# Optimization experiments

Measured on AMD Instinct MI355X. Metric: run time of the kernel, lower is better.

The kernel has to match this reference:

```python
import jax, jax.numpy as jnp
import numpy as np

EPS = 1e-5

def _ln(x, g, b):
    m = jnp.mean(x, -1, keepdims=True)
    v = jnp.mean((x - m) ** 2, -1, keepdims=True)
    return (x - m) * jax.lax.rsqrt(v + EPS) * g + b

def _lstm(x, Wih, Whh, bih, bhh):
    # x: [B, T, D]; torch gate order i, f, g, o; h0 = c0 = 0
    B = x.shape[0]
    H = Whh.shape[1]
    h0 = jnp.zeros((B, H), x.dtype)
    c0 = jnp.zeros((B, H), x.dtype)
    bias = bih + bhh
    def step(carry, xt):
        h, c = carry
        gates = xt @ Wih.T + h @ Whh.T + bias  # [B, 4H]
        i, f, g, o = jnp.split(gates, 4, axis=-1)
        c = jax.nn.sigmoid(f) * c + jax.nn.sigmoid(i) * jnp.tanh(g)
        h = jax.nn.sigmoid(o) * jnp.tanh(c)
        return (h, c), h
    _, hs = jax.lax.scan(step, (h0, c0), jnp.swapaxes(x, 0, 1))
    return jnp.swapaxes(hs, 0, 1)  # [B, T, H]

def setup_inputs() -> dict:
    key = jax.random.key(0)
    ks = jax.random.split(key, 20)
    N, C, F, T = 4, 64, 256, 256
    D, H = 128, 32  # LSTM in/out
    s = 0.05
    inp = {
        "inputs": jax.random.normal(ks[0], (N, C, F, T, 2), jnp.float32),
        "ln1_g": jnp.ones((D,), jnp.float32), "ln1_b": jnp.zeros((D,), jnp.float32),
        "Wih_q": s * jax.random.normal(ks[1], (4 * H, D), jnp.float32),
        "Whh_q": s * jax.random.normal(ks[2], (4 * H, H), jnp.float32),
        "bih_q": s * jax.random.normal(ks[3], (4 * H,), jnp.float32),
        "bhh_q": s * jax.random.normal(ks[4], (4 * H,), jnp.float32),
        "Wih_k": s * jax.random.normal(ks[5], (4 * H, D), jnp.float32),
        "Whh_k": s * jax.random.normal(ks[6], (4 * H, H), jnp.float32),
        "bih_k": s * jax.random.normal(ks[7], (4 * H,), jnp.float32),
        "bhh_k": s * jax.random.normal(ks[8], (4 * H,), jnp.float32),
        "Wih_v": s * jax.random.normal(ks[9], (4 * H, D), jnp.float32),
        "Whh_v": s * jax.random.normal(ks[10], (4 * H, H), jnp.float32),
        "bih_v": s * jax.random.normal(ks[11], (4 * H,), jnp.float32),
        "bhh_v": s * jax.random.normal(ks[12], (4 * H,), jnp.float32),
        "ln2_g": jnp.ones((H,), jnp.float32), "ln2_b": jnp.zeros((H,), jnp.float32),
        "Wr": s * jax.random.normal(ks[13], (C, H // 2), jnp.float32),
        "br": s * jax.random.normal(ks[14], (C,), jnp.float32),
        "Wi": s * jax.random.normal(ks[15], (C, H // 2), jnp.float32),
        "bi": s * jax.random.normal(ks[16], (C,), jnp.float32),
        "ln3_g": jnp.ones((C,), jnp.float32), "ln3_b": jnp.zeros((C,), jnp.float32),
        "prelu_a": jnp.full((1,), 0.25, jnp.float32),
    }
    return inp

def reference(inputs, ln1_g, ln1_b,
              Wih_q, Whh_q, bih_q, bhh_q,
              Wih_k, Whh_k, bih_k, bhh_k,
              Wih_v, Whh_v, bih_v, bhh_v,
              ln2_g, ln2_b, Wr, br, Wi, bi,
              ln3_g, ln3_b, prelu_a):
    N, C, F, T, ri = inputs.shape
    # [N,C,F,T,2] -> [N*F, T, C, 2] -> concat real/imag -> [N*F, T, 2C]
    x4 = jnp.transpose(inputs, (0, 2, 3, 1, 4)).reshape(N * F, T, C, ri)
    x = jnp.concatenate([x4[..., 0], x4[..., 1]], axis=-1)  # [B, T, 128]
    # Self_Attention_T_RICAT (single head)
    xn = _ln(x, ln1_g, ln1_b)
    q = _lstm(xn, Wih_q, Whh_q, bih_q, bhh_q)  # [B, T, 32]
    k = _lstm(xn, Wih_k, Whh_k, bih_k, bhh_k)
    v = _lstm(xn, Wih_v, Whh_v, bih_v, bhh_v)
    energy = jnp.einsum('btf,bsf->bts', q, k) / 4.0  # / 16**0.5
    mask = jnp.tril(jnp.ones((T, T), x.dtype))
    attn = jax.nn.softmax(energy * mask, axis=-1)  # multiplicative mask, as in source
    wv = jnp.einsum('bts,bsf->btf', attn, v)  # [B, T, 32]
    out = _ln(wv, ln2_g, ln2_b)
    # complex-valued linear fusion
    xr, xi = jnp.split(out, 2, axis=-1)  # [B, T, 16] each
    lr_r = xr @ Wr.T + br
    li_i = xi @ Wi.T + bi
    lr_i = xi @ Wr.T + br
    li_r = xr @ Wi.T + bi
    out_real = (lr_r - li_i).reshape(N, F, T, C).transpose(0, 3, 1, 2)  # [N,C,F,T]
    out_imag = (lr_i + li_r).reshape(N, F, T, C).transpose(0, 3, 1, 2)
    outs = jnp.stack([out_real, out_imag], axis=-1)  # [N,C,F,T,2]
    outs_t = jnp.swapaxes(outs, 1, 4)  # [N,2,F,T,C]
    outs = jnp.swapaxes(_ln(outs_t, ln3_g, ln3_b), 1, 4)
    outs = jnp.where(outs >= 0, outs, prelu_a[0] * outs)  # PReLU (eval mode, dropout=identity)
    return outs + inputs
```

## Files before the change

### kernel.cpp

```cpp
#include <hip/hip_runtime.h>
#include <hip/hip_bf16.h>
#include <stddef.h>


typedef __bf16 bf16x8 __attribute__((ext_vector_type(8)));
typedef float f32x4 __attribute__((ext_vector_type(4)));

__device__ __forceinline__ ushort f2bf(float x) {
    uint u = __builtin_bit_cast(uint, x);
    uint r = (u + 0x7fffu + ((u >> 16) & 1u)) >> 16;
    return (ushort)r;
}

__device__ __forceinline__ float fsig(float x) {
    return __builtin_amdgcn_rcpf(1.f + __expf(-x));
}
__device__ __forceinline__ float ftanh(float x) {
    return 1.f - 2.f * __builtin_amdgcn_rcpf(__expf(2.f * x) + 1.f);
}
__device__ __forceinline__ float wredsum(float v) {
#pragma unroll
    for (int off = 32; off; off >>= 1) v += __shfl_xor(v, off);
    return v;
}
__device__ __forceinline__ float hredsum(float v) {
#pragma unroll
    for (int off = 16; off; off >>= 1) v += __shfl_xor(v, off);
    return v;
}

__global__ __launch_bounds__(256) void k_prep(const float* __restrict__ in,
                                              const float* __restrict__ g1,
                                              const float* __restrict__ b1,
                                              ushort* __restrict__ xn) {
    __shared__ float xl[32][129];
    const int n = blockIdx.z, f = blockIdx.y, t0 = blockIdx.x * 32;
    const int tid = threadIdx.x;
    const int c = tid >> 2, q = tid & 3;
    const float* src = in + ((size_t)(n * 64 + c) * 256 + f) * 512 + t0 * 2 + q * 16;
#pragma unroll
    for (int e = 0; e < 4; ++e) {
        float4 v4 = *(const float4*)(src + e * 4);
        int dt = q * 8 + e * 2;
        xl[dt][c]          = v4.x;
        xl[dt][c + 64]     = v4.y;
        xl[dt + 1][c]      = v4.z;
        xl[dt + 1][c + 64] = v4.w;
    }
    __syncthreads();
    const int lane = tid & 63, w = tid >> 6;
    const int b = n * 256 + f;
#pragma unroll 1
    for (int r = 0; r < 8; ++r) {
        int dt = w * 8 + r;
        float a = xl[dt][lane], bb = xl[dt][lane + 64];
        float s = wredsum(a + bb);
        float mean = s * 0.0078125f;
        float da = a - mean, db = bb - mean;
        float var = wredsum(da * da + db * db) * 0.0078125f;
        float inv = __builtin_amdgcn_rsqf(var + 1e-5f);
        size_t base = ((size_t)b * 256 + (t0 + dt)) * 128;
        xn[base + lane]      = f2bf(da * inv * g1[lane] + b1[lane]);
        xn[base + lane + 64] = f2bf(db * inv * g1[lane + 64] + b1[lane + 64]);
    }
}

__global__ __launch_bounds__(256) void k_gemm(const ushort* __restrict__ xn,
                                              const float* __restrict__ Wq,
                                              const float* __restrict__ Wk,
                                              const float* __restrict__ Wv,
                                              const float* __restrict__ bihq, const float* __restrict__ bhhq,
                                              const float* __restrict__ bihk, const float* __restrict__ bhhk,
                                              const float* __restrict__ bihv, const float* __restrict__ bhhv,
                                              ushort* __restrict__ gx) {
    __shared__ ushort a_lds[128 * 136];
    __shared__ ushort w_lds[128 * 136];
    const int tid = threadIdx.x;
    const int m0 = blockIdx.x * 128;

#pragma unroll
    for (int p = 0; p < 8; ++p) {
        int idx = p * 256 + tid;
        int r = idx >> 4, c = idx & 15;
        *(uint4*)&a_lds[r * 136 + c * 8] =
            *(const uint4*)(xn + (size_t)(m0 + r) * 128 + c * 8);
    }

    const int w = tid >> 6, lane = tid & 63;
    const int wr = w >> 1, wc = w & 1;
    const int row16 = lane & 15, koct = lane >> 4;

#pragma unroll 1
    for (int l = 0; l < 3; ++l) {
        const float* W   = (l == 0) ? Wq   : (l == 1) ? Wk   : Wv;
        const float* bih = (l == 0) ? bihq : (l == 1) ? bihk : bihv;
        const float* bhh = (l == 0) ? bhhq : (l == 1) ? bhhk : bhhv;
        __syncthreads();
#pragma unroll
        for (int p = 0; p < 8; ++p) {
            int idx = p * 256 + tid;
            int r = idx >> 4, c = idx & 15;
            const float* wp = W + (size_t)r * 128 + c * 8;
            float4 wa = *(const float4*)wp;
            float4 wb = *(const float4*)(wp + 4);
            union { ushort u[8]; uint4 v; } pk;
            pk.u[0] = f2bf(wa.x); pk.u[1] = f2bf(wa.y); pk.u[2] = f2bf(wa.z); pk.u[3] = f2bf(wa.w);
            pk.u[4] = f2bf(wb.x); pk.u[5] = f2bf(wb.y); pk.u[6] = f2bf(wb.z); pk.u[7] = f2bf(wb.w);
            *(uint4*)&w_lds[r * 136 + c * 8] = pk.v;
        }
        __syncthreads();

        f32x4 acc[4][4];
#pragma unroll
        for (int mi = 0; mi < 4; ++mi)
#pragma unroll
            for (int ni = 0; ni < 4; ++ni) acc[mi][ni] = (f32x4){0.f, 0.f, 0.f, 0.f};

#pragma unroll
        for (int ki = 0; ki < 4; ++ki) {
            bf16x8 af[4], bfr[4];
#pragma unroll
            for (int mi = 0; mi < 4; ++mi)
                af[mi] = *(const bf16x8*)&a_lds[(wr * 64 + mi * 16 + row16) * 136 + ki * 32 + koct * 8];
#pragma unroll
            for (int ni = 0; ni < 4; ++ni)
                bfr[ni] = *(const bf16x8*)&w_lds[(wc * 64 + ni * 16 + row16) * 136 + ki * 32 + koct * 8];
#pragma unroll
            for (int mi = 0; mi < 4; ++mi)
#pragma unroll
                for (int ni = 0; ni < 4; ++ni)
                    acc[mi][ni] = __builtin_amdgcn_mfma_f32_16x16x32_bf16(af[mi], bfr[ni], acc[mi][ni], 0, 0, 0);
        }
        __syncthreads();

#pragma unroll
        for (int ni = 0; ni < 4; ++ni) {
            int g = wc * 64 + ni * 16 + row16;
            float bsv = bih[g] + bhh[g];
            int j = g & 31, gi = g >> 5;
            int s = j * 4 + gi;
#pragma unroll
            for (int mi = 0; mi < 4; ++mi)
#pragma unroll
                for (int q = 0; q < 4; ++q) {
                    int ml = wr * 64 + mi * 16 + koct * 4 + q;
                    w_lds[ml * 136 + s] = f2bf(acc[mi][ni][q] + bsv);
                }
        }
        __syncthreads();
#pragma unroll
        for (int p = 0; p < 8; ++p) {
            int idx = p * 256 + tid;
            int r = idx >> 4, cchunk = idx & 15;
            *(uint4*)&gx[(size_t)(m0 + r) * 384 + l * 128 + cchunk * 8] =
                *(const uint4*)&w_lds[r * 136 + cchunk * 8];
        }
    }
}

__global__ __launch_bounds__(128, 1) void k_lstm(const ushort* __restrict__ gx,
                                                 const float* __restrict__ Whq,
                                                 const float* __restrict__ Whk,
                                                 const float* __restrict__ Whv,
                                                 ushort* __restrict__ qkv) {
    __shared__ ushort H[2][16][40];
    const int tid = threadIdx.x;
    const int w = tid >> 6, lane = tid & 63;
    const int r16 = lane & 15, koct = lane >> 4;
    const int l = blockIdx.x >> 6, bgrp = blockIdx.x & 63;
    const int b = bgrp * 16 + r16;
    const float* Wh = (l == 0) ? Whq : (l == 1) ? Whk : Whv;

    bf16x8 wf[4];
#pragma unroll
    for (int gg = 0; gg < 4; ++gg) {
        int g = 4 * w + gg;
        int jA = 8 * (r16 >> 2) + g;
        int giA = r16 & 3;
        const float* wp = Wh + (size_t)(giA * 32 + jA) * 32 + koct * 8;
        float4 wa = *(const float4*)wp;
        float4 wb = *(const float4*)(wp + 4);
        union { ushort u[8]; bf16x8 v; } pk;
        pk.u[0] = f2bf(wa.x); pk.u[1] = f2bf(wa.y); pk.u[2] = f2bf(wa.z); pk.u[3] = f2bf(wa.w);
        pk.u[4] = f2bf(wb.x); pk.u[5] = f2bf(wb.y); pk.u[6] = f2bf(wb.z); pk.u[7] = f2bf(wb.w);
        wf[gg] = pk.v;
    }

    const ushort* gp = gx + (size_t)b * 98304 + l * 128 + koct * 32 + w * 16;
    uint4 pf[4][2];
#pragma unroll
    for (int tt = 0; tt < 4; ++tt) {
        pf[tt][0] = *(const uint4*)(gp + (size_t)tt * 384);
        pf[tt][1] = *(const uint4*)(gp + (size_t)tt * 384 + 8);
    }

    for (int i = tid; i < 320; i += 128) ((uint*)&H[0][0][0])[i] = 0;
    __syncthreads();

    float cst[4] = {0.f, 0.f, 0.f, 0.f};
    ushort* outp = qkv + ((size_t)(l * 1024 + b)) * 8192 + koct * 8 + w * 4;

#pragma unroll 4
    for (int t = 0; t < 256; ++t) {
        const int sl = t & 3;
        const int p = t & 1;
        bf16x8 hf = *(const bf16x8*)&H[p][r16][koct * 8];

        uint u[8];
        u[0] = pf[sl][0].x; u[1] = pf[sl][0].y; u[2] = pf[sl][0].z; u[3] = pf[sl][0].w;
        u[4] = pf[sl][1].x; u[5] = pf[sl][1].y; u[6] = pf[sl][1].z; u[7] = pf[sl][1].w;
        pf[sl][0] = *(const uint4*)(gp + (size_t)(t + 4) * 384);
        pf[sl][1] = *(const uint4*)(gp + (size_t)(t + 4) * 384 + 8);

        f32x4 acc[4];
#pragma unroll
        for (int gg = 0; gg < 4; ++gg)
#pragma unroll
            for (int q = 0; q < 4; ++q) {
                int v = gg * 4 + q;
                uint w32 = u[v >> 1];
                acc[gg][q] = __builtin_bit_cast(float, (v & 1) ? (w32 & 0xffff0000u) : (w32 << 16));
            }
#pragma unroll
        for (int gg = 0; gg < 4; ++gg)
            acc[gg] = __builtin_amdgcn_mfma_f32_16x16x32_bf16(wf[gg], hf, acc[gg], 0, 0, 0);

        float hv[4];
#pragma unroll
        for (int gg = 0; gg < 4; ++gg) {
            float gi = acc[gg][0], gf = acc[gg][1], gg2 = acc[gg][2], go = acc[gg][3];
            float cN = fsig(gf) * cst[gg] + fsig(gi) * ftanh(gg2);
            cst[gg] = cN;
            hv[gg] = fsig(go) * ftanh(cN);
        }
        uint2 hp;
        __asm__ volatile("v_cvt_pk_bf16_f32 %0, %1, %2" : "=v"(hp.x) : "v"(hv[0]), "v"(hv[1]));
        __asm__ volatile("v_cvt_pk_bf16_f32 %0, %1, %2" : "=v"(hp.y) : "v"(hv[2]), "v"(hv[3]));
        *(uint2*)&H[p ^ 1][r16][koct * 8 + w * 4] = hp;
        *(uint2*)(outp + (size_t)t * 32) = hp;
        __syncthreads();
    }
}

__global__ __launch_bounds__(256) void k_attn(const ushort* __restrict__ qkvb,
                                              float* __restrict__ wvout) {
    __shared__ ushort k_sw[256 * 32];
    __shared__ ushort vt_sw[32 * 256];
    __shared__ ushort p_sw[4][16 * 256];
    const int tid = threadIdx.x, w = tid >> 6, lane = tid & 63;
    const int b = blockIdx.x;
    const ushort* qb = qkvb + (size_t)b * 8192;
    const ushort* kb = qkvb + 8388608 + (size_t)b * 8192;
    const ushort* vb = qkvb + 16777216 + (size_t)b * 8192;
#pragma unroll
    for (int p = 0; p < 4; ++p) {
        int idx = p * 256 + tid;
        int s = idx >> 2, cc = idx & 3;
        uint4 kv = *(const uint4*)(kb + s * 32 + cc * 8);
        int cK = cc ^ ((s >> 1) & 3);
        *(uint4*)&k_sw[s * 32 + cK * 8] = kv;
        uint4 vv = *(const uint4*)(vb + s * 32 + cc * 8);
        union { uint4 v; ushort u[8]; } un; un.v = vv;
#pragma unroll
        for (int e = 0; e < 8; ++e) {
            int row = cc * 8 + e;
            vt_sw[row * 256 + (((s >> 3) ^ (row & 7)) << 3) + (s & 7)] = un.u[e];
        }
    }
    __syncthreads();
    const int r16 = lane & 15, koct = lane >> 4;
    ushort* pw = p_sw[w];
    bf16x8 qf[4];
#pragma unroll
    for (int i = 0; i < 4; ++i) {
        int t = (w * 4 + i) * 16 + r16;
        qf[i] = *(const bf16x8*)(qb + t * 32 + koct * 8);
    }
#pragma unroll 1
    for (int i = 0; i < 4; ++i) {
        const int tb = (w * 4 + i) * 16;
        f32x4 acc[16];
#pragma unroll
        for (int st = 0; st < 16; ++st) acc[st] = (f32x4){0.f, 0.f, 0.f, 0.f};
#pragma unroll
        for (int st = 0; st < 16; ++st) {
            int s = st * 16 + r16;
            int cK = koct ^ ((s >> 1) & 3);
            bf16x8 kf = *(const bf16x8*)&k_sw[s * 32 + cK * 8];
            acc[st] = __builtin_amdgcn_mfma_f32_16x16x32_bf16(qf[i], kf, acc[st], 0, 0, 0);
        }
        float mx[4] = {-1e30f, -1e30f, -1e30f, -1e30f};
#pragma unroll
        for (int st = 0; st < 16; ++st) {
            int s = st * 16 + r16;
#pragma unroll
            for (int q = 0; q < 4; ++q) {
                int t = tb + koct * 4 + q;
                float v = (s <= t) ? acc[st][q] * 0.25f : 0.f;
                acc[st][q] = v;
                mx[q] = fmaxf(mx[q], v);
            }
        }
#pragma unroll
        for (int off = 1; off < 16; off <<= 1)
#pragma unroll
            for (int q = 0; q < 4; ++q) mx[q] = fmaxf(mx[q], __shfl_xor(mx[q], off));
        float sm[4] = {0.f, 0.f, 0.f, 0.f};
#pragma unroll
        for (int st = 0; st < 16; ++st)
#pragma unroll
            for (int q = 0; q < 4; ++q) {
                float p = __expf(acc[st][q] - mx[q]);
                acc[st][q] = p; sm[q] += p;
            }
#pragma unroll
        for (int off = 1; off < 16; off <<= 1)
#pragma unroll
            for (int q = 0; q < 4; ++q) sm[q] += __shfl_xor(sm[q], off);
        float rs[4];
#pragma unroll
        for (int q = 0; q < 4; ++q) rs[q] = __builtin_amdgcn_rcpf(sm[q]);
#pragma unroll
        for (int st = 0; st < 16; ++st) {
            int schunk = st * 2 + (r16 >> 3), sl = r16 & 7;
#pragma unroll
            for (int q = 0; q < 4; ++q) {
                int tl = koct * 4 + q;
                pw[tl * 256 + ((schunk ^ (tl & 7)) << 3) + sl] = f2bf(acc[st][q] * rs[q]);
            }
        }
        __asm__ volatile("s_waitcnt lgkmcnt(0)" ::: "memory");
        f32x4 oa[2];
        oa[0] = (f32x4){0.f, 0.f, 0.f, 0.f};
        oa[1] = (f32x4){0.f, 0.f, 0.f, 0.f};
#pragma unroll
        for (int ks = 0; ks < 8; ++ks) {
            int kc = ks * 4 + koct;
            bf16x8 pa = *(const bf16x8*)&pw[r16 * 256 + ((kc ^ (r16 & 7)) << 3)];
#pragma unroll
            for (int n = 0; n < 2; ++n) {
                int row = n * 16 + r16;
                bf16x8 vf = *(const bf16x8*)&vt_sw[row * 256 + ((kc ^ (row & 7)) << 3)];
                oa[n] = __builtin_amdgcn_mfma_f32_16x16x32_bf16(pa, vf, oa[n], 0, 0, 0);
            }
        }
#pragma unroll
        for (int n = 0; n < 2; ++n)
#pragma unroll
            for (int q = 0; q < 4; ++q)
                wvout[((size_t)b * 256 + tb + koct * 4 + q) * 32 + n * 16 + r16] = oa[n][q];
    }
}

__global__ __launch_bounds__(256) void k_post(const float* __restrict__ wv,
                                              const float* __restrict__ in,
                                              const float* __restrict__ g2,
                                              const float* __restrict__ b2,
                                              const float* __restrict__ Wr,
                                              const float* __restrict__ br,
                                              const float* __restrict__ Wi,
                                              const float* __restrict__ bi,
                                              const float* __restrict__ g3,
                                              const float* __restrict__ b3,
                                              const float* __restrict__ pa,
                                              float* __restrict__ outp) {
    __shared__ float xv[32][36];
    __shared__ float out_s[64][65];
    const int tid = threadIdx.x;
    const int n = blockIdx.z, f = blockIdx.y, t0 = blockIdx.x * 32;
    const int b = n * 256 + f;
    const int lane = tid & 63, w = tid >> 6;
    const int r16 = lane & 15, koct = lane >> 4;
    const int tt = w & 1, ri = w >> 1;

    for (int idx = tid; idx < 1024; idx += 256) {
        int dt = idx >> 5, j = idx & 31;
        xv[dt][j] = wv[((size_t)b * 256 + t0 + dt) * 32 + j];
    }

    bf16x8 bfr[4];
    float bias_v[4], g3v[4], b3v[4];
    const int kofs = (koct < 2) ? koct * 8 : (koct - 2) * 8;
#pragma unroll
    for (int ct = 0; ct < 4; ++ct) {
        int c = ct * 16 + r16;
        const float* srcW = (ri == 0) ? ((koct < 2) ? Wr : Wi)
                                      : ((koct < 2) ? Wi : Wr);
        float sgn = (ri == 0 && koct >= 2) ? -1.f : 1.f;
        float4 wa = *(const float4*)(srcW + c * 16 + kofs);
        float4 wb = *(const float4*)(srcW + c * 16 + kofs + 4);
        union { ushort u[8]; bf16x8 v; } pk;
        pk.u[0] = f2bf(sgn * wa.x); pk.u[1] = f2bf(sgn * wa.y);
        pk.u[2] = f2bf(sgn * wa.z); pk.u[3] = f2bf(sgn * wa.w);
        pk.u[4] = f2bf(sgn * wb.x); pk.u[5] = f2bf(sgn * wb.y);
        pk.u[6] = f2bf(sgn * wb.z); pk.u[7] = f2bf(sgn * wb.w);
        bfr[ct] = pk.v;
        bias_v[ct] = (ri == 0) ? (br[c] - bi[c]) : (br[c] + bi[c]);
        g3v[ct] = g3[c];
        b3v[ct] = b3[c];
    }
    const float alpha = pa[0];
    __syncthreads();

#pragma unroll 1
    for (int r = 0; r < 4; ++r) {
        int dt = w * 8 + r * 2 + (lane >> 5);
        int j = lane & 31;
        float v = xv[dt][j];
        float mean = hredsum(v) * 0.03125f;
        float d = v - mean;
        float var = hredsum(d * d) * 0.03125f;
        float inv = __builtin_amdgcn_rsqf(var + 1e-5f);
        xv[dt][j] = d * inv * g2[j] + b2[j];
    }
    __syncthreads();

    const float* xrow = &xv[tt * 16 + r16][koct * 8];
    float4 a0 = *(const float4*)xrow;
    float4 a1 = *(const float4*)(xrow + 4);
    uint4 ap;
    __asm__ volatile("v_cvt_pk_bf16_f32 %0, %1, %2" : "=v"(ap.x) : "v"(a0.x), "v"(a0.y));
    __asm__ volatile("v_cvt_pk_bf16_f32 %0, %1, %2" : "=v"(ap.y) : "v"(a0.z), "v"(a0.w));
    __asm__ volatile("v_cvt_pk_bf16_f32 %0, %1, %2" : "=v"(ap.z) : "v"(a1.x), "v"(a1.y));
    __asm__ volatile("v_cvt_pk_bf16_f32 %0, %1, %2" : "=v"(ap.w) : "v"(a1.z), "v"(a1.w));
    bf16x8 af = __builtin_bit_cast(bf16x8, ap);

    f32x4 acc[4];
#pragma unroll
    for (int ct = 0; ct < 4; ++ct) {
        acc[ct] = (f32x4){0.f, 0.f, 0.f, 0.f};
        acc[ct] = __builtin_amdgcn_mfma_f32_16x16x32_bf16(af, bfr[ct], acc[ct], 0, 0, 0);
    }

    float val[4][4];
    float s[4] = {0.f, 0.f, 0.f, 0.f}, sq[4] = {0.f, 0.f, 0.f, 0.f};
#pragma unroll
    for (int ct = 0; ct < 4; ++ct)
#pragma unroll
        for (int q = 0; q < 4; ++q) {
            float v = acc[ct][q] + bias_v[ct];
            val[ct][q] = v;
            s[q] += v;
            sq[q] += v * v;
        }
#pragma unroll
    for (int off = 1; off < 16; off <<= 1)
#pragma unroll
        for (int q = 0; q < 4; ++q) {
            s[q]  += __shfl_xor(s[q], off);
            sq[q] += __shfl_xor(sq[q], off);
        }
#pragma unroll
    for (int q = 0; q < 4; ++q) {
        float m = s[q] * 0.015625f;
        float var = fmaxf(sq[q] * 0.015625f - m * m, 0.f);
        float inv = __builtin_amdgcn_rsqf(var + 1e-5f);
        int t2 = (tt * 16 + koct * 4 + q) * 2 + ri;
#pragma unroll
        for (int ct = 0; ct < 4; ++ct) {
            float nv = (val[ct][q] - m) * inv * g3v[ct] + b3v[ct];
            nv = (nv >= 0.f) ? nv : alpha * nv;
            out_s[ct * 16 + r16][t2] = nv;
        }
    }
    __syncthreads();

    const int cc = tid >> 2, q = tid & 3;
    size_t base = ((size_t)(n * 64 + cc) * 256 + f) * 512 + t0 * 2 + q * 16;
#pragma unroll
    for (int e = 0; e < 4; ++e) {
        float4 iv = *(const float4*)(in + base + e * 4);
        int k0 = q * 16 + e * 4;
        float4 ov;
        ov.x = out_s[cc][k0]     + iv.x;
        ov.y = out_s[cc][k0 + 1] + iv.y;
        ov.z = out_s[cc][k0 + 2] + iv.z;
        ov.w = out_s[cc][k0 + 3] + iv.w;
        *(float4*)(outp + base + e * 4) = ov;
    }
}

extern "C" void kernel_launch(void* const* d_in, const int* in_sizes, int n_in,
                              void* d_out, int out_size, void* d_ws, size_t ws_size,
                              hipStream_t stream) {
    const float* in   = (const float*)d_in[0];
    const float* g1   = (const float*)d_in[1];
    const float* b1   = (const float*)d_in[2];
    const float* Wq   = (const float*)d_in[3];
    const float* Whq  = (const float*)d_in[4];
    const float* bihq = (const float*)d_in[5];
    const float* bhhq = (const float*)d_in[6];
    const float* Wk   = (const float*)d_in[7];
    const float* Whk  = (const float*)d_in[8];
    const float* bihk = (const float*)d_in[9];
    const float* bhhk = (const float*)d_in[10];
    const float* Wv   = (const float*)d_in[11];
    const float* Whv  = (const float*)d_in[12];
    const float* bihv = (const float*)d_in[13];
    const float* bhhv = (const float*)d_in[14];
    const float* g2   = (const float*)d_in[15];
    const float* b2   = (const float*)d_in[16];
    const float* Wr   = (const float*)d_in[17];
    const float* br   = (const float*)d_in[18];
    const float* Wi   = (const float*)d_in[19];
    const float* bi   = (const float*)d_in[20];
    const float* g3   = (const float*)d_in[21];
    const float* b3   = (const float*)d_in[22];
    const float* pa   = (const float*)d_in[23];
    float* outp = (float*)d_out;

    ushort* gxb  = (ushort*)d_ws;
    ushort* xnb  = (ushort*)((char*)d_ws + 201326592);
    ushort* qkvb = (ushort*)((char*)d_ws + 268435456);
    float*  wvb  = (float*)((char*)d_ws + 318767104);

    k_prep<<<dim3(8, 256, 4), dim3(256), 0, stream>>>(in, g1, b1, xnb);
    k_gemm<<<dim3(2048), dim3(256), 0, stream>>>(xnb, Wq, Wk, Wv,
                                                 bihq, bhhq, bihk, bhhk, bihv, bhhv, gxb);
    k_lstm<<<dim3(192), dim3(128), 0, stream>>>(gxb, Whq, Whk, Whv, qkvb);
    k_attn<<<dim3(1024), dim3(256), 0, stream>>>(qkvb, wvb);
    k_post<<<dim3(8, 256, 4), dim3(256), 0, stream>>>(wvb, in, g2, b2,
                                                      Wr, br, Wi, bi, g3, b3, pa, outp);
}
```

Measured before the change: 471.9 us.

## Fuse input LayerNorm and transpose into the gate GEMM kernel

Drops the separate prep kernel. Each GEMM block now loads its 128 time steps of raw input, transposes them through LDS (reusing the weight buffer), applies LayerNorm and writes bf16 straight into the A tile in LDS. This removes the global write and re-read of the normalized bf16 activations (about 67 MB) and one kernel launch. In exchange the GEMM blocks do extra serialized load/normalize phases with more barriers before the MFMA work.

```diff
diff --git a/kernel.cpp b/kernel.cpp
--- a/kernel.cpp
+++ b/kernel.cpp
@@ -29,43 +29,9 @@
     return v;
 }
 
-__global__ __launch_bounds__(256) void k_prep(const float* __restrict__ in,
+__global__ __launch_bounds__(256) void k_gemm(const float* __restrict__ in,
                                               const float* __restrict__ g1,
                                               const float* __restrict__ b1,
-                                              ushort* __restrict__ xn) {
-    __shared__ float xl[32][129];
-    const int n = blockIdx.z, f = blockIdx.y, t0 = blockIdx.x * 32;
-    const int tid = threadIdx.x;
-    const int c = tid >> 2, q = tid & 3;
-    const float* src = in + ((size_t)(n * 64 + c) * 256 + f) * 512 + t0 * 2 + q * 16;
-#pragma unroll
-    for (int e = 0; e < 4; ++e) {
-        float4 v4 = *(const float4*)(src + e * 4);
-        int dt = q * 8 + e * 2;
-        xl[dt][c]          = v4.x;
-        xl[dt][c + 64]     = v4.y;
-        xl[dt + 1][c]      = v4.z;
-        xl[dt + 1][c + 64] = v4.w;
-    }
-    __syncthreads();
-    const int lane = tid & 63, w = tid >> 6;
-    const int b = n * 256 + f;
-#pragma unroll 1
-    for (int r = 0; r < 8; ++r) {
-        int dt = w * 8 + r;
-        float a = xl[dt][lane], bb = xl[dt][lane + 64];
-        float s = wredsum(a + bb);
-        float mean = s * 0.0078125f;
-        float da = a - mean, db = bb - mean;
-        float var = wredsum(da * da + db * db) * 0.0078125f;
-        float inv = __builtin_amdgcn_rsqf(var + 1e-5f);
-        size_t base = ((size_t)b * 256 + (t0 + dt)) * 128;
-        xn[base + lane]      = f2bf(da * inv * g1[lane] + b1[lane]);
-        xn[base + lane + 64] = f2bf(db * inv * g1[lane + 64] + b1[lane + 64]);
-    }
-}
-
-__global__ __launch_bounds__(256) void k_gemm(const ushort* __restrict__ xn,
                                               const float* __restrict__ Wq,
                                               const float* __restrict__ Wk,
                                               const float* __restrict__ Wv,
@@ -78,17 +44,46 @@
     const int tid = threadIdx.x;
     const int m0 = blockIdx.x * 128;
 
-#pragma unroll
-    for (int p = 0; p < 8; ++p) {
-        int idx = p * 256 + tid;
-        int r = idx >> 4, c = idx & 15;
-        *(uint4*)&a_lds[r * 136 + c * 8] =
-            *(const uint4*)(xn + (size_t)(m0 + r) * 128 + c * 8);
-    }
-
     const int w = tid >> 6, lane = tid & 63;
     const int wr = w >> 1, wc = w & 1;
     const int row16 = lane & 15, koct = lane >> 4;
+
+    {
+        const int b_seq = blockIdx.x >> 1;
+        const int t0 = (blockIdx.x & 1) * 128;
+        const int n = b_seq >> 8, f = b_seq & 255;
+        float (*xl)[129] = (float(*)[129])w_lds;
+        const int c = tid >> 2, q = tid & 3;
+#pragma unroll 1
+        for (int tc = 0; tc < 4; ++tc) {
+            const float* src = in + ((size_t)(n * 64 + c) * 256 + f) * 512
+                                  + (size_t)(t0 + tc * 32) * 2 + q * 16;
+#pragma unroll
+            for (int e = 0; e < 4; ++e) {
+                float4 v4 = *(const float4*)(src + e * 4);
+                int dt = q * 8 + e * 2;
+                xl[dt][c]          = v4.x;
+                xl[dt][c + 64]     = v4.y;
+                xl[dt + 1][c]      = v4.z;
+                xl[dt + 1][c + 64] = v4.w;
+            }
+            __syncthreads();
+#pragma unroll 1
+            for (int r = 0; r < 8; ++r) {
+                int dt = w * 8 + r;
+                float a = xl[dt][lane], bb = xl[dt][lane + 64];
+                float s = wredsum(a + bb);
+                float mean = s * 0.0078125f;
+                float da = a - mean, db = bb - mean;
+                float var = wredsum(da * da + db * db) * 0.0078125f;
+                float inv = __builtin_amdgcn_rsqf(var + 1e-5f);
+                int row = tc * 32 + dt;
+                a_lds[row * 136 + lane]      = f2bf(da * inv * g1[lane] + b1[lane]);
+                a_lds[row * 136 + lane + 64] = f2bf(db * inv * g1[lane + 64] + b1[lane + 64]);
+            }
+            __syncthreads();
+        }
+    }
 
 #pragma unroll 1
     for (int l = 0; l < 3; ++l) {
@@ -510,12 +505,10 @@
     float* outp = (float*)d_out;
 
     ushort* gxb  = (ushort*)d_ws;
-    ushort* xnb  = (ushort*)((char*)d_ws + 201326592);
     ushort* qkvb = (ushort*)((char*)d_ws + 268435456);
     float*  wvb  = (float*)((char*)d_ws + 318767104);
 
-    k_prep<<<dim3(8, 256, 4), dim3(256), 0, stream>>>(in, g1, b1, xnb);
-    k_gemm<<<dim3(2048), dim3(256), 0, stream>>>(xnb, Wq, Wk, Wv,
+    k_gemm<<<dim3(2048), dim3(256), 0, stream>>>(in, g1, b1, Wq, Wk, Wv,
                                                  bihq, bhhq, bihk, bhhk, bihv, bhhv, gxb);
     k_lstm<<<dim3(192), dim3(128), 0, stream>>>(gxb, Whq, Whk, Whv, qkvb);
     k_attn<<<dim3(1024), dim3(256), 0, stream>>>(qkvb, wvb);
```

New measurement: 483.6 us. +2.5%, slower.
